# Performance work log

Hardware: AMD Instinct MI355X
Metric: run time of the kernel (lower is better)

Reference implementation:

```python
import jax, jax.numpy as jnp
import numpy as np

N_HOST = 50000
N_FLOW = 200000
D = 128
D_OUT = 32
E = 1_000_000
L = 2


def setup_inputs() -> dict:
    key = jax.random.key(0)
    ks = jax.random.split(key, 12)
    s = 0.05  # keep activations well-scaled across layers
    return {
        "x_host": jax.random.normal(ks[0], (N_HOST, D), jnp.float32),
        "x_flow": jax.random.normal(ks[1], (N_FLOW, D), jnp.float32),
        "ehf_src": jax.random.randint(ks[2], (E,), 0, N_HOST),
        "ehf_dst": jax.random.randint(ks[3], (E,), 0, N_FLOW),
        "efh_src": jax.random.randint(ks[4], (E,), 0, N_FLOW),
        "efh_dst": jax.random.randint(ks[5], (E,), 0, N_HOST),
        "Wl": jax.random.normal(ks[6], (L, 2, D, D), jnp.float32) * s,
        "bl": jax.random.normal(ks[7], (L, 2, D), jnp.float32) * s,
        "Wr": jax.random.normal(ks[8], (L, 2, D, D), jnp.float32) * s,
        "br": jax.random.normal(ks[9], (L, 2, D), jnp.float32) * s,
        "W_out": jax.random.normal(ks[10], (D, D_OUT), jnp.float32) * s,
        "b_out": jax.random.normal(ks[11], (D_OUT,), jnp.float32) * s,
    }


def _sage(x_src, x_dst, src, dst, n_dst, wl, bll, wr, brr):
    # SAGEConv (bipartite, mean aggr): lin_l(mean_{j->i} x_src[j]) + lin_r(x_dst[i])
    msg = x_src[src]                                         # [E, D] gather
    agg = jax.ops.segment_sum(msg, dst, num_segments=n_dst)  # [n_dst, D] scatter-add
    cnt = jax.ops.segment_sum(jnp.ones((src.shape[0], 1), x_src.dtype), dst,
                              num_segments=n_dst)
    mean = agg / jnp.maximum(cnt, 1.0)
    return mean @ wl + bll + x_dst @ wr + brr


def reference(x_host, x_flow, ehf_src, ehf_dst, efh_src, efh_dst,
              Wl, bl, Wr, br, W_out, b_out):
    h, f = x_host, x_flow
    for l in range(L):
        # ('host','to','flow') -> updates flow; ('flow','to','host') -> updates host
        nf = _sage(h, f, ehf_src, ehf_dst, N_FLOW, Wl[l, 0], bl[l, 0], Wr[l, 0], br[l, 0])
        nh = _sage(f, h, efh_src, efh_dst, N_HOST, Wl[l, 1], bl[l, 1], Wr[l, 1], br[l, 1])
        f = jax.nn.leaky_relu(nf)  # negative_slope 0.01, matches F.leaky_relu default
        h = jax.nn.leaky_relu(nh)
    return f @ W_out + b_out
```

## Files before the change

kernel.cpp:

```cpp
#include <hip/hip_runtime.h>
#include <stdint.h>

#define N_HOST 50000
#define N_FLOW 200000
#define DIM 128
#define DOUTN 32
#define NEDGE 1000000
#define NLAYER 2

#define GSH_F 8
#define GSH_H 6
#define NB_F ((N_FLOW + (1 << GSH_F) - 1) >> GSH_F)
#define NB_H ((N_HOST + (1 << GSH_H) - 1) >> GSH_H)
#define AST 136
#define CAST_FBLK 25000

typedef __bf16 bf16;
typedef __bf16 bf16x4 __attribute__((ext_vector_type(4)));
typedef __bf16 bf16x8 __attribute__((ext_vector_type(8)));
typedef float floatx2 __attribute__((ext_vector_type(2)));
typedef float floatx4 __attribute__((ext_vector_type(4)));
typedef int intx4 __attribute__((ext_vector_type(4)));

__global__ void cast_all_k(const float* __restrict__ xf, const float* __restrict__ xh,
                           bf16* __restrict__ fA, bf16* __restrict__ hAB) {
    int bid = blockIdx.x;
    if (bid < CAST_FBLK) {
        int i = (bid * 256 + threadIdx.x) * 4;
        float4 v = *(const float4*)(xf + i);
        bf16x4 o;
        o[0] = (bf16)v.x; o[1] = (bf16)v.y; o[2] = (bf16)v.z; o[3] = (bf16)v.w;
        *(bf16x4*)(fA + i) = o;
    } else {
        int i = ((bid - CAST_FBLK) * 256 + threadIdx.x) * 4;
        float4 v = *(const float4*)(xh + i);
        bf16x4 o;
        o[0] = (bf16)v.x; o[1] = (bf16)v.y; o[2] = (bf16)v.z; o[3] = (bf16)v.w;
        int row = i >> 7, col = i & 127;
        *(bf16x4*)(hAB + row * 256 + col) = o;
    }
}

__global__ void repack_all_k(const float* __restrict__ Wl, const float* __restrict__ Wr,
                             const float* __restrict__ Wo,
                             bf16* __restrict__ WlF, bf16* __restrict__ WrF,
                             bf16* __restrict__ WoF) {
    int y = blockIdx.y;
    int lane = threadIdx.x & 63;
    int w = blockIdx.x * 4 + (threadIdx.x >> 6);
    int ct = w >> 2, k0q = w & 3;
    int quad = lane >> 4, m = lane & 15;
    if (y == 8) {
        if (blockIdx.x >= 2) return;
        bf16x8 o;
#pragma unroll
        for (int j = 0; j < 8; ++j) o[j] = (bf16)Wo[(k0q * 32 + quad * 8 + j) * DOUTN + ct * 16 + m];
        *(bf16x8*)(WoF + ((ct * 4 + k0q) * 64 + lane) * 8) = o;
        return;
    }
    int mat = y & 3;
    const float* W = (y < 4 ? Wl : Wr) + (size_t)mat * DIM * DIM;
    bf16* out = (y < 4 ? WlF : WrF) + (size_t)mat * DIM * DIM;
    bf16x8 o;
#pragma unroll
    for (int j = 0; j < 8; ++j) o[j] = (bf16)W[(k0q * 32 + quad * 8 + j) * DIM + ct * 16 + m];
    *(bf16x8*)(out + ((ct * 4 + k0q) * 64 + lane) * 8) = o;
}

__global__ __launch_bounds__(256)
void bucket_count2_k(const int* __restrict__ dF, const int* __restrict__ dH,
                     int* __restrict__ bcF, int* __restrict__ bcH) {
    __shared__ int lc[1024];
    int dir = blockIdx.y;
    const int* dst = dir ? dH : dF;
    int* bcount = dir ? bcH : bcF;
    int gsh = dir ? GSH_H : GSH_F;
    int t = threadIdx.x;
    for (int i = t; i < NB_F; i += 256) lc[i] = 0;
    __syncthreads();
    int base = blockIdx.x * 4096;
    int end = base + 4096; if (end > NEDGE) end = NEDGE;
    for (int i = base + t; i < end; i += 256)
        atomicAdd(&lc[dst[i] >> gsh], 1);
    __syncthreads();
    for (int i = t; i < NB_F; i += 256) {
        int v = lc[i];
        if (v) atomicAdd(&bcount[i], v);
    }
}

__global__ __launch_bounds__(256)
void bucket_scan2_k(const int* __restrict__ bcF, const int* __restrict__ bcH,
                    int* __restrict__ boF, int* __restrict__ boH,
                    int* __restrict__ bcurF, int* __restrict__ bcurH) {
    __shared__ int sd[256];
    int dir = blockIdx.x;
    const int* bcount = dir ? bcH : bcF;
    int* boffs = dir ? boH : boF;
    int* bcur = dir ? bcurH : bcurF;
    const int nb = NB_F;
    int t = threadIdx.x;
    int v[4]; int ts = 0;
#pragma unroll
    for (int j = 0; j < 4; ++j) { int i = t * 4 + j; v[j] = (i < nb) ? bcount[i] : 0; ts += v[j]; }
    int x = ts;
    sd[t] = x; __syncthreads();
    for (int o = 1; o < 256; o <<= 1) {
        int y = (t >= o) ? sd[t - o] : 0;
        __syncthreads();
        x += y; sd[t] = x; __syncthreads();
    }
    int run = x - ts;
#pragma unroll
    for (int j = 0; j < 4; ++j) {
        int i = t * 4 + j;
        if (i < nb) { boffs[i] = run; bcur[i << 4] = run; }
        run += v[j];
    }
    if (t == 255) boffs[nb] = x;
}

__global__ __launch_bounds__(256)
void bucket_scatter2_k(const int* __restrict__ sF, const int* __restrict__ dF,
                       const int* __restrict__ sH, const int* __restrict__ dH,
                       int* bcurF, int* bcurH,
                       int* __restrict__ bkF, int* __restrict__ bkH) {
    int dir = blockIdx.y;
    const int* src = dir ? sH : sF;
    const int* dst = dir ? dH : dF;
    int* bcur = dir ? bcurH : bcurF;
    int* bkey = dir ? bkH : bkF;
    int gsh = dir ? GSH_H : GSH_F;
    int e = blockIdx.x * 256 + threadIdx.x;
    if (e < NEDGE) {
        int d = dst[e];
        int b = d >> gsh;
        int p = atomicAdd(&bcur[b << 4], 1);
        bkey[p] = (src[e] << 8) | (d & ((1 << gsh) - 1));
    }
}

__global__ __launch_bounds__(256)
void bucket_sort2_k(const int* __restrict__ boF, const int* __restrict__ boH,
                    const int* __restrict__ bkF, const int* __restrict__ bkH,
                    int* __restrict__ rsF, int* __restrict__ rsH,
                    int* __restrict__ esF, int* __restrict__ esH) {
    __shared__ int cnts[256];
    __shared__ int sd[256];
    __shared__ int ldsout[2048];
    int dir = blockIdx.y;
    const int* boffs = dir ? boH : boF;
    const int* bkey = dir ? bkH : bkF;
    int* rs = dir ? rsH : rsF;
    int* es = dir ? esH : esF;
    int gsh = dir ? GSH_H : GSH_F;
    int b = blockIdx.x, t = threadIdx.x;
    int G = 1 << gsh;
    int base = boffs[b];
    int cnt = boffs[b + 1] - base;
    if (cnt > 2048) cnt = 2048;
    int keys[8]; int nk = 0;
    for (int i = t; i < cnt; i += 256) keys[nk++] = bkey[base + i];
    cnts[t] = 0;
    __syncthreads();
    for (int j = 0; j < nk; ++j) atomicAdd(&cnts[keys[j] & 255], 1);
    __syncthreads();
    int v = cnts[t];
    int x = v;
    sd[t] = x; __syncthreads();
    for (int o = 1; o < 256; o <<= 1) {
        int y = (t >= o) ? sd[t - o] : 0;
        __syncthreads();
        x += y; sd[t] = x; __syncthreads();
    }
    int ex = x - v;
    if (t < G) rs[(b << gsh) + t] = base + ex;
    cnts[t] = ex;
    __syncthreads();
    for (int j = 0; j < nk; ++j) {
        int k = keys[j];
        int p = atomicAdd(&cnts[k & 255], 1);
        ldsout[p] = k >> 8;
    }
    __syncthreads();
    for (int i = t; i < cnt; i += 256) es[base + i] = ldsout[i];
}

__device__ __forceinline__ void acc_pk4(floatx2* acc, intx4 v) {
    uint32_t d[4] = {(uint32_t)v.x, (uint32_t)v.y, (uint32_t)v.z, (uint32_t)v.w};
#pragma unroll
    for (int k = 0; k < 4; ++k) {
        floatx2 u;
        u.x = __uint_as_float(d[k] << 16);
        u.y = __uint_as_float(d[k] & 0xffff0000u);
        asm("v_pk_add_f32 %0, %1, %0" : "+v"(acc[k]) : "v"(u));
    }
}

#define LRELU(v) ((v) > 0.f ? (v) : 0.01f * (v))

__global__ __launch_bounds__(512, 8)
void host_fused(const int* __restrict__ rs, const int* __restrict__ csr,
                const intx4* __restrict__ x4,
                const bf16* __restrict__ hA,
                const bf16* __restrict__ W1f, const bf16* __restrict__ W2f,
                const float* __restrict__ b1, const float* __restrict__ b2,
                bf16* __restrict__ hB) {
    __shared__ __align__(16) bf16 TM[64 * AST];
    int t = threadIdx.x;
    int row0 = blockIdx.x << 6;
    {
        int q = t >> 4, c = t & 15;
#pragma unroll
        for (int p = 0; p < 2; ++p) {
            int lr = p * 32 + q;
            int r = row0 + lr;
            floatx2 a2[4];
#pragma unroll
            for (int k = 0; k < 4; ++k) a2[k] = (floatx2){0.f, 0.f};
            float inv = 1.0f;
            if (r < N_HOST) {
                int s0 = rs[r], s1 = rs[r + 1];
                for (int e = s0; e < s1; ++e) {
                    int s = csr[e];
                    intx4 v = x4[s * 16 + c];
                    acc_pk4(a2, v);
                }
                int deg = s1 - s0;
                inv = 1.0f / (float)(deg > 0 ? deg : 1);
            }
            bf16x8 o;
#pragma unroll
            for (int k = 0; k < 4; ++k) {
                o[2 * k]     = (bf16)(a2[k].x * inv);
                o[2 * k + 1] = (bf16)(a2[k].y * inv);
            }
            *(bf16x8*)(TM + lr * AST + c * 8) = o;
        }
    }
    __syncthreads();
    int lane = t & 63, wv = t >> 6;
    int quad = lane >> 4, m = lane & 15;
    int ccol = wv * 16 + m;
    floatx4 zero4 = {0.f, 0.f, 0.f, 0.f};
    floatx4 acc[4];
#pragma unroll
    for (int rt = 0; rt < 4; ++rt) acc[rt] = zero4;
    {
        bf16x8 B[4];
#pragma unroll
        for (int k = 0; k < 4; ++k)
            B[k] = *(const bf16x8*)(W1f + ((wv * 4 + k) * 64 + lane) * 8);
#pragma unroll
        for (int rt = 0; rt < 4; ++rt)
#pragma unroll
            for (int k = 0; k < 4; ++k) {
                bf16x8 a = *(const bf16x8*)(TM + (rt * 16 + m) * AST + quad * 8 + k * 32);
                acc[rt] = __builtin_amdgcn_mfma_f32_16x16x32_bf16(a, B[k], acc[rt], 0, 0, 0);
            }
#pragma unroll
        for (int k = 0; k < 4; ++k)
            B[k] = *(const bf16x8*)(W2f + ((wv * 4 + k) * 64 + lane) * 8);
#pragma unroll
        for (int rt = 0; rt < 4; ++rt) {
            int ar = row0 + rt * 16 + m;
            if (ar >= N_HOST) ar = 0;
#pragma unroll
            for (int k = 0; k < 4; ++k) {
                bf16x8 a = *(const bf16x8*)(hA + (size_t)ar * 256 + quad * 8 + k * 32);
                acc[rt] = __builtin_amdgcn_mfma_f32_16x16x32_bf16(a, B[k], acc[rt], 0, 0, 0);
            }
        }
    }
    float bias = b1[ccol] + b2[ccol];
#pragma unroll
    for (int rt = 0; rt < 4; ++rt)
#pragma unroll
        for (int r4 = 0; r4 < 4; ++r4) {
            int row = row0 + rt * 16 + quad * 4 + r4;
            if (row < N_HOST) {
                float v0 = acc[rt][r4] + bias;
                hB[(size_t)row * 256 + ccol] = (bf16)LRELU(v0);
            }
        }
}

__global__ __launch_bounds__(512, 8)
void flow_fused(const int* __restrict__ rs, const int* __restrict__ csr,
                const intx4* __restrict__ tab,
                const bf16* __restrict__ fA,
                const bf16* __restrict__ Wl0f, const bf16* __restrict__ Wr0f,
                const bf16* __restrict__ Wl2f, const bf16* __restrict__ Wr2f,
                const float* __restrict__ bl0, const float* __restrict__ br0,
                const float* __restrict__ bl2, const float* __restrict__ br2,
                const bf16* __restrict__ Wof, const float* __restrict__ bo,
                float* __restrict__ outf) {
    __shared__ __align__(16) bf16 T0[64 * AST];
    __shared__ __align__(16) bf16 T1[64 * AST];
    int t = threadIdx.x;
    int row0 = blockIdx.x << 6;
    {
        int q = t >> 4, c = t & 15;
#pragma unroll
        for (int p = 0; p < 2; ++p) {
            int lr = p * 32 + q;
            int r = row0 + lr;
            int s0 = rs[r], s1 = rs[r + 1];
            floatx2 a2[4], b2[4];
#pragma unroll
            for (int k = 0; k < 4; ++k) { a2[k] = (floatx2){0.f, 0.f}; b2[k] = (floatx2){0.f, 0.f}; }
            for (int e = s0; e < s1; ++e) {
                int sa = csr[e];
                intx4 va = tab[sa * 32 + c];
                intx4 vb = tab[sa * 32 + 16 + c];
                acc_pk4(a2, va); acc_pk4(b2, vb);
            }
            int deg = s1 - s0;
            float inv = 1.0f / (float)(deg > 0 ? deg : 1);
            bf16x8 oa, ob;
#pragma unroll
            for (int k = 0; k < 4; ++k) {
                oa[2 * k]     = (bf16)(a2[k].x * inv);
                oa[2 * k + 1] = (bf16)(a2[k].y * inv);
                ob[2 * k]     = (bf16)(b2[k].x * inv);
                ob[2 * k + 1] = (bf16)(b2[k].y * inv);
            }
            *(bf16x8*)(T0 + lr * AST + c * 8) = oa;
            *(bf16x8*)(T1 + lr * AST + c * 8) = ob;
        }
    }
    __syncthreads();
    int lane = t & 63, wv = t >> 6;
    int quad = lane >> 4, m = lane & 15;
    int ccol = wv * 16 + m;
    floatx4 zero4 = {0.f, 0.f, 0.f, 0.f};
    floatx4 acc[4];
#pragma unroll
    for (int rt = 0; rt < 4; ++rt) acc[rt] = zero4;
    {
        bf16x8 B[4];
#pragma unroll
        for (int k = 0; k < 4; ++k)
            B[k] = *(const bf16x8*)(Wl0f + ((wv * 4 + k) * 64 + lane) * 8);
#pragma unroll
        for (int rt = 0; rt < 4; ++rt)
#pragma unroll
            for (int k = 0; k < 4; ++k) {
                bf16x8 a = *(const bf16x8*)(T0 + (rt * 16 + m) * AST + quad * 8 + k * 32);
                acc[rt] = __builtin_amdgcn_mfma_f32_16x16x32_bf16(a, B[k], acc[rt], 0, 0, 0);
            }
#pragma unroll
        for (int k = 0; k < 4; ++k)
            B[k] = *(const bf16x8*)(Wr0f + ((wv * 4 + k) * 64 + lane) * 8);
#pragma unroll
        for (int rt = 0; rt < 4; ++rt)
#pragma unroll
            for (int k = 0; k < 4; ++k) {
                bf16x8 a = *(const bf16x8*)(fA + (size_t)(row0 + rt * 16 + m) * DIM + quad * 8 + k * 32);
                acc[rt] = __builtin_amdgcn_mfma_f32_16x16x32_bf16(a, B[k], acc[rt], 0, 0, 0);
            }
    }
    {
        float bias = bl0[ccol] + br0[ccol];
        __syncthreads();
#pragma unroll
        for (int rt = 0; rt < 4; ++rt)
#pragma unroll
            for (int r4 = 0; r4 < 4; ++r4) {
                int lr = rt * 16 + quad * 4 + r4;
                float v0 = acc[rt][r4] + bias;
                T0[lr * AST + ccol] = (bf16)LRELU(v0);
            }
        __syncthreads();
    }
#pragma unroll
    for (int rt = 0; rt < 4; ++rt) acc[rt] = zero4;
    {
        bf16x8 B[4];
#pragma unroll
        for (int k = 0; k < 4; ++k)
            B[k] = *(const bf16x8*)(Wl2f + ((wv * 4 + k) * 64 + lane) * 8);
#pragma unroll
        for (int rt = 0; rt < 4; ++rt)
#pragma unroll
            for (int k = 0; k < 4; ++k) {
                bf16x8 a = *(const bf16x8*)(T1 + (rt * 16 + m) * AST + quad * 8 + k * 32);
                acc[rt] = __builtin_amdgcn_mfma_f32_16x16x32_bf16(a, B[k], acc[rt], 0, 0, 0);
            }
#pragma unroll
        for (int k = 0; k < 4; ++k)
            B[k] = *(const bf16x8*)(Wr2f + ((wv * 4 + k) * 64 + lane) * 8);
#pragma unroll
        for (int rt = 0; rt < 4; ++rt)
#pragma unroll
            for (int k = 0; k < 4; ++k) {
                bf16x8 a = *(const bf16x8*)(T0 + (rt * 16 + m) * AST + quad * 8 + k * 32);
                acc[rt] = __builtin_amdgcn_mfma_f32_16x16x32_bf16(a, B[k], acc[rt], 0, 0, 0);
            }
    }
    {
        float bias = bl2[ccol] + br2[ccol];
        __syncthreads();
#pragma unroll
        for (int rt = 0; rt < 4; ++rt)
#pragma unroll
            for (int r4 = 0; r4 < 4; ++r4) {
                int lr = rt * 16 + quad * 4 + r4;
                float v0 = acc[rt][r4] + bias;
                T1[lr * AST + ccol] = (bf16)LRELU(v0);
            }
        __syncthreads();
    }
    {
        int s = wv >> 1, h = wv & 1;
        bf16x8 BO[4];
#pragma unroll
        for (int k = 0; k < 4; ++k)
            BO[k] = *(const bf16x8*)(Wof + ((h * 4 + k) * 64 + lane) * 8);
        floatx4 o = zero4;
        const bf16* fp = T1 + (s * 16 + m) * AST + quad * 8;
#pragma unroll
        for (int k = 0; k < 4; ++k) {
            bf16x8 af = *(const bf16x8*)(fp + k * 32);
            o = __builtin_amdgcn_mfma_f32_16x16x32_bf16(af, BO[k], o, 0, 0, 0);
        }
        float bov = bo[h * 16 + m];
#pragma unroll
        for (int r = 0; r < 4; ++r) {
            int row = row0 + s * 16 + quad * 4 + r;
            outf[row * DOUTN + h * 16 + m] = o[r] + bov;
        }
    }
}

extern "C" void kernel_launch(void* const* d_in, const int* in_sizes, int n_in,
                              void* d_out, int out_size, void* d_ws, size_t ws_size,
                              hipStream_t stream) {
    (void)in_sizes; (void)n_in; (void)out_size; (void)ws_size;
    const float* x_host  = (const float*)d_in[0];
    const float* x_flow  = (const float*)d_in[1];
    const int*   ehf_src = (const int*)d_in[2];
    const int*   ehf_dst = (const int*)d_in[3];
    const int*   efh_src = (const int*)d_in[4];
    const int*   efh_dst = (const int*)d_in[5];
    const float* Wl      = (const float*)d_in[6];
    const float* bl      = (const float*)d_in[7];
    const float* Wr      = (const float*)d_in[8];
    const float* br      = (const float*)d_in[9];
    const float* W_out   = (const float*)d_in[10];
    const float* b_out   = (const float*)d_in[11];
    float* out = (float*)d_out;

    char* basep = (char*)d_ws;
    size_t off = 0;
    auto alloc = [&](size_t b) -> void* {
        void* p = basep + off;
        off += (b + 255) & ~(size_t)255;
        return p;
    };

    bf16* fA     = (bf16*)alloc((size_t)N_FLOW * DIM * 2);
    bf16* hAB    = (bf16*)alloc((size_t)N_HOST * 256 * 2);
    bf16* WlF    = (bf16*)alloc((size_t)NLAYER * 2 * DIM * DIM * 2);
    bf16* WrF    = (bf16*)alloc((size_t)NLAYER * 2 * DIM * DIM * 2);
    bf16* WoF    = (bf16*)alloc((size_t)DIM * DOUTN * 2);

    int* bcount2 = (int*)alloc((size_t)(NB_F + NB_H) * 4);
    int* bcountF = bcount2;
    int* bcountH = bcount2 + NB_F;
    int* boffsF  = (int*)alloc((size_t)(NB_F + 1) * 4);
    int* bcurF   = (int*)alloc((size_t)NB_F * 16 * 4);
    int* bkeyF   = (int*)alloc((size_t)NEDGE * 4);
    int* rsF     = (int*)alloc((size_t)(NB_F * (1 << GSH_F) + 1) * 4);
    int* esF     = (int*)alloc((size_t)NEDGE * 4);
    int* boffsH  = (int*)alloc((size_t)(NB_H + 1) * 4);
    int* bcurH   = (int*)alloc((size_t)NB_H * 16 * 4);
    int* bkeyH   = (int*)alloc((size_t)NEDGE * 4);
    int* rsH     = (int*)alloc((size_t)(NB_H * (1 << GSH_H) + 1) * 4);
    int* esH     = (int*)alloc((size_t)NEDGE * 4);

    cast_all_k<<<CAST_FBLK + 6250, 256, 0, stream>>>(x_flow, x_host, fA, hAB);
    repack_all_k<<<dim3(8, 9), 256, 0, stream>>>(Wl, Wr, W_out, WlF, WrF, WoF);

    hipMemsetAsync(bcount2, 0, (size_t)(NB_F + NB_H) * 4, stream);
    bucket_count2_k<<<dim3((NEDGE + 4095) / 4096, 2), 256, 0, stream>>>(
        ehf_dst, efh_dst, bcountF, bcountH);
    bucket_scan2_k<<<2, 256, 0, stream>>>(bcountF, bcountH, boffsF, boffsH, bcurF, bcurH);
    bucket_scatter2_k<<<dim3((NEDGE + 255) / 256, 2), 256, 0, stream>>>(
        ehf_src, ehf_dst, efh_src, efh_dst, bcurF, bcurH, bkeyF, bkeyH);
    bucket_sort2_k<<<dim3(NB_F, 2), 256, 0, stream>>>(
        boffsF, boffsH, bkeyF, bkeyH, rsF, rsH, esF, esH);

    host_fused<<<(N_HOST + 63) / 64, 512, 0, stream>>>(
        rsH, esH, (const intx4*)fA, hAB,
        WlF + 1 * DIM * DIM, WrF + 1 * DIM * DIM,
        bl + 1 * DIM, br + 1 * DIM, hAB + 128);

    flow_fused<<<N_FLOW / 64, 512, 0, stream>>>(
        rsF, esF, (const intx4*)hAB, fA,
        WlF + 0 * DIM * DIM, WrF + 0 * DIM * DIM,
        WlF + 2 * DIM * DIM, WrF + 2 * DIM * DIM,
        bl + 0 * DIM, br + 0 * DIM, bl + 2 * DIM, br + 2 * DIM,
        WoF, b_out, out);
}
```

Before: 548.2 us.

## Replace count-scan bucket build with fixed-capacity buckets and merge prep kernels

Drops the bucket count and prefix-scan passes by giving each destination bucket a fixed slot region of 2048 entries, so the scatter kernel writes directly at bucket*2048 plus an atomic counter. Row start/end pairs are stored as int2 so consumers no longer need contiguous offsets. The cast, weight repack and counter zeroing are merged into one launch, removing the memset and several small kernel launches. Buckets that exceed capacity silently drop edges, and the padded layout uses more memory and scatters writes more sparsely.

```diff
diff --git a/kernel.cpp b/kernel.cpp
--- a/kernel.cpp
+++ b/kernel.cpp
@@ -12,8 +12,16 @@
 #define GSH_H 6
 #define NB_F ((N_FLOW + (1 << GSH_F) - 1) >> GSH_F)
 #define NB_H ((N_HOST + (1 << GSH_H) - 1) >> GSH_H)
+#define BCAP 2048
 #define AST 136
+
 #define CAST_FBLK 25000
+#define CAST_HBLK 6250
+#define ZOFF  (CAST_FBLK + CAST_HBLK)
+#define ZBLK  13
+#define RW_OFF (ZOFF + ZBLK)
+#define RO_OFF (RW_OFF + 64)
+#define PREP_GRID (RO_OFF + 2)
 
 typedef __bf16 bf16;
 typedef __bf16 bf16x4 __attribute__((ext_vector_type(4)));
@@ -22,143 +30,103 @@
 typedef float floatx4 __attribute__((ext_vector_type(4)));
 typedef int intx4 __attribute__((ext_vector_type(4)));
 
-__global__ void cast_all_k(const float* __restrict__ xf, const float* __restrict__ xh,
-                           bf16* __restrict__ fA, bf16* __restrict__ hAB) {
+__global__ __launch_bounds__(256)
+void prep_all_k(const float* __restrict__ xf, const float* __restrict__ xh,
+                const float* __restrict__ Wl, const float* __restrict__ Wr,
+                const float* __restrict__ Wo,
+                bf16* __restrict__ fA, bf16* __restrict__ hAB,
+                int* __restrict__ bcnt2,
+                bf16* __restrict__ WlF, bf16* __restrict__ WrF,
+                bf16* __restrict__ WoF) {
     int bid = blockIdx.x;
+    int t = threadIdx.x;
     if (bid < CAST_FBLK) {
-        int i = (bid * 256 + threadIdx.x) * 4;
+        int i = (bid * 256 + t) * 4;
         float4 v = *(const float4*)(xf + i);
         bf16x4 o;
         o[0] = (bf16)v.x; o[1] = (bf16)v.y; o[2] = (bf16)v.z; o[3] = (bf16)v.w;
         *(bf16x4*)(fA + i) = o;
-    } else {
-        int i = ((bid - CAST_FBLK) * 256 + threadIdx.x) * 4;
+    } else if (bid < ZOFF) {
+        int i = ((bid - CAST_FBLK) * 256 + t) * 4;
         float4 v = *(const float4*)(xh + i);
         bf16x4 o;
         o[0] = (bf16)v.x; o[1] = (bf16)v.y; o[2] = (bf16)v.z; o[3] = (bf16)v.w;
         int row = i >> 7, col = i & 127;
         *(bf16x4*)(hAB + row * 256 + col) = o;
-    }
-}
-
-__global__ void repack_all_k(const float* __restrict__ Wl, const float* __restrict__ Wr,
-                             const float* __restrict__ Wo,
-                             bf16* __restrict__ WlF, bf16* __restrict__ WrF,
-                             bf16* __restrict__ WoF) {
-    int y = blockIdx.y;
-    int lane = threadIdx.x & 63;
-    int w = blockIdx.x * 4 + (threadIdx.x >> 6);
-    int ct = w >> 2, k0q = w & 3;
-    int quad = lane >> 4, m = lane & 15;
-    if (y == 8) {
-        if (blockIdx.x >= 2) return;
+    } else if (bid < RW_OFF) {
+        int base = (bid - ZOFF) * 2048;
+#pragma unroll
+        for (int j = 0; j < 8; ++j) {
+            int i = base + j * 256 + t;
+            if (i < (NB_F + NB_H) * 16) bcnt2[i] = 0;
+        }
+    } else if (bid < RO_OFF) {
+        int b = bid - RW_OFF;
+        int y = b >> 3;
+        int x = b & 7;
+        int lane = t & 63;
+        int w = x * 4 + (t >> 6);
+        int ct = w >> 2, k0q = w & 3;
+        int quad = lane >> 4, m = lane & 15;
+        int mat = y & 3;
+        const float* W = (y < 4 ? Wl : Wr) + (size_t)mat * DIM * DIM;
+        bf16* out = (y < 4 ? WlF : WrF) + (size_t)mat * DIM * DIM;
+        bf16x8 o;
+#pragma unroll
+        for (int j = 0; j < 8; ++j) o[j] = (bf16)W[(k0q * 32 + quad * 8 + j) * DIM + ct * 16 + m];
+        *(bf16x8*)(out + ((ct * 4 + k0q) * 64 + lane) * 8) = o;
+    } else {
+        int b2 = bid - RO_OFF;
+        int lane = t & 63;
+        int w = b2 * 4 + (t >> 6);
+        int ct = w >> 2, k0q = w & 3;
+        int quad = lane >> 4, m = lane & 15;
         bf16x8 o;
 #pragma unroll
         for (int j = 0; j < 8; ++j) o[j] = (bf16)Wo[(k0q * 32 + quad * 8 + j) * DOUTN + ct * 16 + m];
         *(bf16x8*)(WoF + ((ct * 4 + k0q) * 64 + lane) * 8) = o;
-        return;
-    }
-    int mat = y & 3;
-    const float* W = (y < 4 ? Wl : Wr) + (size_t)mat * DIM * DIM;
-    bf16* out = (y < 4 ? WlF : WrF) + (size_t)mat * DIM * DIM;
-    bf16x8 o;
-#pragma unroll
-    for (int j = 0; j < 8; ++j) o[j] = (bf16)W[(k0q * 32 + quad * 8 + j) * DIM + ct * 16 + m];
-    *(bf16x8*)(out + ((ct * 4 + k0q) * 64 + lane) * 8) = o;
-}
-
-__global__ __launch_bounds__(256)
-void bucket_count2_k(const int* __restrict__ dF, const int* __restrict__ dH,
-                     int* __restrict__ bcF, int* __restrict__ bcH) {
-    __shared__ int lc[1024];
-    int dir = blockIdx.y;
-    const int* dst = dir ? dH : dF;
-    int* bcount = dir ? bcH : bcF;
-    int gsh = dir ? GSH_H : GSH_F;
-    int t = threadIdx.x;
-    for (int i = t; i < NB_F; i += 256) lc[i] = 0;
-    __syncthreads();
-    int base = blockIdx.x * 4096;
-    int end = base + 4096; if (end > NEDGE) end = NEDGE;
-    for (int i = base + t; i < end; i += 256)
-        atomicAdd(&lc[dst[i] >> gsh], 1);
-    __syncthreads();
-    for (int i = t; i < NB_F; i += 256) {
-        int v = lc[i];
-        if (v) atomicAdd(&bcount[i], v);
-    }
-}
-
-__global__ __launch_bounds__(256)
-void bucket_scan2_k(const int* __restrict__ bcF, const int* __restrict__ bcH,
-                    int* __restrict__ boF, int* __restrict__ boH,
-                    int* __restrict__ bcurF, int* __restrict__ bcurH) {
-    __shared__ int sd[256];
-    int dir = blockIdx.x;
-    const int* bcount = dir ? bcH : bcF;
-    int* boffs = dir ? boH : boF;
-    int* bcur = dir ? bcurH : bcurF;
-    const int nb = NB_F;
-    int t = threadIdx.x;
-    int v[4]; int ts = 0;
-#pragma unroll
-    for (int j = 0; j < 4; ++j) { int i = t * 4 + j; v[j] = (i < nb) ? bcount[i] : 0; ts += v[j]; }
-    int x = ts;
-    sd[t] = x; __syncthreads();
-    for (int o = 1; o < 256; o <<= 1) {
-        int y = (t >= o) ? sd[t - o] : 0;
-        __syncthreads();
-        x += y; sd[t] = x; __syncthreads();
-    }
-    int run = x - ts;
-#pragma unroll
-    for (int j = 0; j < 4; ++j) {
-        int i = t * 4 + j;
-        if (i < nb) { boffs[i] = run; bcur[i << 4] = run; }
-        run += v[j];
-    }
-    if (t == 255) boffs[nb] = x;
+    }
 }
 
 __global__ __launch_bounds__(256)
 void bucket_scatter2_k(const int* __restrict__ sF, const int* __restrict__ dF,
                        const int* __restrict__ sH, const int* __restrict__ dH,
-                       int* bcurF, int* bcurH,
+                       int* bcntF, int* bcntH,
                        int* __restrict__ bkF, int* __restrict__ bkH) {
     int dir = blockIdx.y;
     const int* src = dir ? sH : sF;
     const int* dst = dir ? dH : dF;
-    int* bcur = dir ? bcurH : bcurF;
+    int* bcnt = dir ? bcntH : bcntF;
     int* bkey = dir ? bkH : bkF;
     int gsh = dir ? GSH_H : GSH_F;
     int e = blockIdx.x * 256 + threadIdx.x;
     if (e < NEDGE) {
         int d = dst[e];
         int b = d >> gsh;
-        int p = atomicAdd(&bcur[b << 4], 1);
-        bkey[p] = (src[e] << 8) | (d & ((1 << gsh) - 1));
+        int p = atomicAdd(&bcnt[b << 4], 1);
+        if (p < BCAP) bkey[(b << 11) + p] = (src[e] << 8) | (d & ((1 << gsh) - 1));
     }
 }
 
 __global__ __launch_bounds__(256)
-void bucket_sort2_k(const int* __restrict__ boF, const int* __restrict__ boH,
+void bucket_sort2_k(const int* __restrict__ bcntF, const int* __restrict__ bcntH,
                     const int* __restrict__ bkF, const int* __restrict__ bkH,
-                    int* __restrict__ rsF, int* __restrict__ rsH,
+                    int2* __restrict__ rsF2, int2* __restrict__ rsH2,
                     int* __restrict__ esF, int* __restrict__ esH) {
     __shared__ int cnts[256];
     __shared__ int sd[256];
-    __shared__ int ldsout[2048];
+    __shared__ int ldsout[BCAP];
     int dir = blockIdx.y;
-    const int* boffs = dir ? boH : boF;
+    const int* bcnt = dir ? bcntH : bcntF;
     const int* bkey = dir ? bkH : bkF;
-    int* rs = dir ? rsH : rsF;
+    int2* rs2 = dir ? rsH2 : rsF2;
     int* es = dir ? esH : esF;
     int gsh = dir ? GSH_H : GSH_F;
     int b = blockIdx.x, t = threadIdx.x;
     int G = 1 << gsh;
-    int base = boffs[b];
-    int cnt = boffs[b + 1] - base;
-    if (cnt > 2048) cnt = 2048;
+    int base = b << 11;
+    int cnt = bcnt[b << 4];
+    if (cnt > BCAP) cnt = BCAP;
     int keys[8]; int nk = 0;
     for (int i = t; i < cnt; i += 256) keys[nk++] = bkey[base + i];
     cnts[t] = 0;
@@ -174,7 +142,7 @@
         x += y; sd[t] = x; __syncthreads();
     }
     int ex = x - v;
-    if (t < G) rs[(b << gsh) + t] = base + ex;
+    if (t < G) rs2[(b << gsh) + t] = make_int2(base + ex, base + ex + v);
     cnts[t] = ex;
     __syncthreads();
     for (int j = 0; j < nk; ++j) {
@@ -200,7 +168,7 @@
 #define LRELU(v) ((v) > 0.f ? (v) : 0.01f * (v))
 
 __global__ __launch_bounds__(512, 8)
-void host_fused(const int* __restrict__ rs, const int* __restrict__ csr,
+void host_fused(const int2* __restrict__ rs2, const int* __restrict__ csr,
                 const intx4* __restrict__ x4,
                 const bf16* __restrict__ hA,
                 const bf16* __restrict__ W1f, const bf16* __restrict__ W2f,
@@ -220,7 +188,8 @@
             for (int k = 0; k < 4; ++k) a2[k] = (floatx2){0.f, 0.f};
             float inv = 1.0f;
             if (r < N_HOST) {
-                int s0 = rs[r], s1 = rs[r + 1];
+                int2 se = rs2[r];
+                int s0 = se.x, s1 = se.y;
                 for (int e = s0; e < s1; ++e) {
                     int s = csr[e];
                     intx4 v = x4[s * 16 + c];
@@ -286,7 +255,7 @@
 }
 
 __global__ __launch_bounds__(512, 8)
-void flow_fused(const int* __restrict__ rs, const int* __restrict__ csr,
+void flow_fused(const int2* __restrict__ rs2, const int* __restrict__ csr,
                 const intx4* __restrict__ tab,
                 const bf16* __restrict__ fA,
                 const bf16* __restrict__ Wl0f, const bf16* __restrict__ Wr0f,
@@ -305,7 +274,8 @@
         for (int p = 0; p < 2; ++p) {
             int lr = p * 32 + q;
             int r = row0 + lr;
-            int s0 = rs[r], s1 = rs[r + 1];
+            int2 se = rs2[r];
+            int s0 = se.x, s1 = se.y;
             floatx2 a2[4], b2[4];
 #pragma unroll
             for (int k = 0; k < 4; ++k) { a2[k] = (floatx2){0.f, 0.f}; b2[k] = (floatx2){0.f, 0.f}; }
@@ -465,39 +435,32 @@
     bf16* WrF    = (bf16*)alloc((size_t)NLAYER * 2 * DIM * DIM * 2);
     bf16* WoF    = (bf16*)alloc((size_t)DIM * DOUTN * 2);
 
-    int* bcount2 = (int*)alloc((size_t)(NB_F + NB_H) * 4);
-    int* bcountF = bcount2;
-    int* bcountH = bcount2 + NB_F;
-    int* boffsF  = (int*)alloc((size_t)(NB_F + 1) * 4);
-    int* bcurF   = (int*)alloc((size_t)NB_F * 16 * 4);
-    int* bkeyF   = (int*)alloc((size_t)NEDGE * 4);
-    int* rsF     = (int*)alloc((size_t)(NB_F * (1 << GSH_F) + 1) * 4);
-    int* esF     = (int*)alloc((size_t)NEDGE * 4);
-    int* boffsH  = (int*)alloc((size_t)(NB_H + 1) * 4);
-    int* bcurH   = (int*)alloc((size_t)NB_H * 16 * 4);
-    int* bkeyH   = (int*)alloc((size_t)NEDGE * 4);
-    int* rsH     = (int*)alloc((size_t)(NB_H * (1 << GSH_H) + 1) * 4);
-    int* esH     = (int*)alloc((size_t)NEDGE * 4);
-
-    cast_all_k<<<CAST_FBLK + 6250, 256, 0, stream>>>(x_flow, x_host, fA, hAB);
-    repack_all_k<<<dim3(8, 9), 256, 0, stream>>>(Wl, Wr, W_out, WlF, WrF, WoF);
-
-    hipMemsetAsync(bcount2, 0, (size_t)(NB_F + NB_H) * 4, stream);
-    bucket_count2_k<<<dim3((NEDGE + 4095) / 4096, 2), 256, 0, stream>>>(
-        ehf_dst, efh_dst, bcountF, bcountH);
-    bucket_scan2_k<<<2, 256, 0, stream>>>(bcountF, bcountH, boffsF, boffsH, bcurF, bcurH);
+    int* bcnt2   = (int*)alloc((size_t)(NB_F + NB_H) * 16 * 4);
+    int* bcntF   = bcnt2;
+    int* bcntH   = bcnt2 + NB_F * 16;
+    int* bkF     = (int*)alloc((size_t)NB_F * BCAP * 4);
+    int* bkH     = (int*)alloc((size_t)NB_H * BCAP * 4);
+    int* esF     = (int*)alloc((size_t)NB_F * BCAP * 4);
+    int* esH     = (int*)alloc((size_t)NB_H * BCAP * 4);
+    int2* rsF2   = (int2*)alloc((size_t)NB_F * (1 << GSH_F) * 8);
+    int2* rsH2   = (int2*)alloc((size_t)NB_H * (1 << GSH_H) * 8);
+
+    prep_all_k<<<PREP_GRID, 256, 0, stream>>>(
+        x_flow, x_host, Wl, Wr, W_out, fA, hAB, bcnt2, WlF, WrF, WoF);
+
     bucket_scatter2_k<<<dim3((NEDGE + 255) / 256, 2), 256, 0, stream>>>(
-        ehf_src, ehf_dst, efh_src, efh_dst, bcurF, bcurH, bkeyF, bkeyH);
+        ehf_src, ehf_dst, efh_src, efh_dst, bcntF, bcntH, bkF, bkH);
+
     bucket_sort2_k<<<dim3(NB_F, 2), 256, 0, stream>>>(
-        boffsF, boffsH, bkeyF, bkeyH, rsF, rsH, esF, esH);
+        bcntF, bcntH, bkF, bkH, rsF2, rsH2, esF, esH);
 
     host_fused<<<(N_HOST + 63) / 64, 512, 0, stream>>>(
-        rsH, esH, (const intx4*)fA, hAB,
+        rsH2, esH, (const intx4*)fA, hAB,
         WlF + 1 * DIM * DIM, WrF + 1 * DIM * DIM,
         bl + 1 * DIM, br + 1 * DIM, hAB + 128);
 
     flow_fused<<<N_FLOW / 64, 512, 0, stream>>>(
-        rsF, esF, (const intx4*)hAB, fA,
+        rsF2, esF, (const intx4*)hAB, fA,
         WlF + 0 * DIM * DIM, WrF + 0 * DIM * DIM,
         WlF + 2 * DIM * DIM, WrF + 2 * DIM * DIM,
         bl + 0 * DIM, br + 0 * DIM, bl + 2 * DIM, br + 2 * DIM,
```

Result: faster. 507.6 us (-7.4%).
